# Performance work log

Hardware: AMD Instinct MI355X
Metric: run time of the kernel (lower is better)

Reference implementation:

```python
import jax, jax.numpy as jnp
import numpy as np

B, S, D, E, F = 4, 2048, 1024, 8, 4096


def setup_inputs() -> dict:
    key = jax.random.key(0)
    k1, k2, k3, k4 = jax.random.split(key, 4)
    x = jax.random.normal(k1, (B, S, D), dtype=jnp.float32)
    Wg = jax.random.normal(k2, (D, E), dtype=jnp.float32) / np.sqrt(D).astype(np.float32)
    w1 = jax.random.normal(k3, (E, D, F), dtype=jnp.float32) / np.sqrt(D).astype(np.float32)
    w2 = jax.random.normal(k4, (E, F, D), dtype=jnp.float32) / np.sqrt(F).astype(np.float32)
    return {"x": x, "Wg": Wg, "w1": w1, "w2": w2, "k": 2}


def reference(x, Wg, w1, w2, k):
    # x: [B, S, D] -> flatten tokens
    b, s, d = x.shape
    e = Wg.shape[1]
    xf = x.reshape(-1, d)                      # [T, D]
    t = xf.shape[0]
    logits = xf @ Wg                           # [T, E] gate logits
    topv, topi = jax.lax.top_k(logits, k)      # [T, k]
    # softmax over the top-k logits in float32, cast back (matches torch impl)
    w = jax.nn.softmax(topv.astype(jnp.float32), axis=-1).astype(x.dtype)
    # dense routing matrix [T, E]: weight for selected experts, 0 elsewhere
    route = jnp.zeros((t, e), dtype=x.dtype).at[jnp.arange(t)[:, None], topi].set(w)
    # per-expert FFN: y_e = gelu(x @ w1[e]) @ w2[e]; combine = sum_e route[:,e] * y_e
    out = jnp.zeros_like(xf)
    for ei in range(e):  # small fixed expert count
        h = jax.nn.gelu(xf @ w1[ei])           # [T, F]
        out = out + route[:, ei:ei + 1] * (h @ w2[ei])
    return out.reshape(b, s, d)
```

## Files before the change

kernel.cpp:

```cpp
#include <hip/hip_runtime.h>
#include <stdint.h>

#define T_TOK   8192
#define DMODEL  1024
#define NEXP    8
#define FFN     4096
#define TASSIGN 16384

typedef unsigned short u16;
typedef __attribute__((ext_vector_type(8))) short short8;
typedef __attribute__((ext_vector_type(8))) u16 u16x8;
typedef __attribute__((ext_vector_type(4))) u16 u16x4;
typedef __attribute__((ext_vector_type(4))) float f32x4;

__device__ __forceinline__ float bf2f(u16 u) {
  union { unsigned int i; float f; } v; v.i = ((unsigned int)u) << 16; return v.f;
}
__device__ __forceinline__ u16 f2bf(float f) {
  union { float f; unsigned int i; } v; v.f = f;
  unsigned int x = v.i;
  x += 0x7fffu + ((x >> 16) & 1u);
  return (u16)(x >> 16);
}
__device__ __forceinline__ float gelu_tanh(float x) {
  float z = 0.7978845608028654f * x * (1.0f + 0.044715f * x * x);
  float t = 1.0f - 2.0f / (__expf(2.0f * z) + 1.0f);
  return 0.5f * x * (1.0f + t);
}
__device__ __forceinline__ void async16(const void* g, void* l) {
  __builtin_amdgcn_global_load_lds((__attribute__((address_space(1))) void*)g,
                                   (__attribute__((address_space(3))) void*)l,
                                   16, 0, 0);
}

__global__ void init_kernel(int* __restrict__ meta) {
  if (threadIdx.x < 32) meta[threadIdx.x] = 0;
}

__global__ void gate_kernel(const float* __restrict__ x, const float* __restrict__ Wg,
                            int* __restrict__ topi, float* __restrict__ topw,
                            int* __restrict__ counts, u16* __restrict__ xb) {
  __shared__ float sWg[DMODEL * NEXP];
  int tid = threadIdx.x;
  for (int i = tid; i < DMODEL * NEXP / 4; i += 256)
    ((float4*)sWg)[i] = ((const float4*)Wg)[i];
  __syncthreads();

  int wave = tid >> 6, lane = tid & 63;
  int t = blockIdx.x * 4 + wave;

  float acc[NEXP] = {0, 0, 0, 0, 0, 0, 0, 0};
  const float* xr = x + (size_t)t * DMODEL;
  u16* xbr = xb + (size_t)t * DMODEL;
  for (int d0 = 0; d0 < DMODEL; d0 += 128) {
    int d = d0 + lane * 2;
    float2 xx = *(const float2*)(xr + d);
    *(uint32_t*)(xbr + d) = (uint32_t)f2bf(xx.x) | ((uint32_t)f2bf(xx.y) << 16);
    const float* g0 = sWg + (size_t)d * NEXP;
#pragma unroll
    for (int e = 0; e < NEXP; e++)
      acc[e] += xx.x * g0[e] + xx.y * g0[NEXP + e];
  }
#pragma unroll
  for (int off = 32; off > 0; off >>= 1)
#pragma unroll
    for (int e = 0; e < NEXP; e++)
      acc[e] += __shfl_xor(acc[e], off, 64);

  if (lane == 0) {
    float v0 = -1e30f, v1 = -1e30f; int i0 = 0, i1 = 0;
#pragma unroll
    for (int e = 0; e < NEXP; e++) {
      float v = acc[e];
      if (v > v0) { v1 = v0; i1 = i0; v0 = v; i0 = e; }
      else if (v > v1) { v1 = v; i1 = e; }
    }
    float e1 = __expf(v1 - v0);
    float s = 1.0f / (1.0f + e1);
    topi[t * 2] = i0; topi[t * 2 + 1] = i1;
    topw[t * 2] = s;  topw[t * 2 + 1] = e1 * s;
    atomicAdd(&counts[i0], 1);
    atomicAdd(&counts[i1], 1);
  }
}

__global__ void scan_kernel(const int* __restrict__ counts, int* __restrict__ offsets,
                            int* __restrict__ cursors) {
  if (threadIdx.x == 0) {
    int s = 0;
    for (int e = 0; e < NEXP; e++) { offsets[e] = s; s += counts[e]; }
    offsets[NEXP] = s;
  }
  if (threadIdx.x < NEXP) cursors[threadIdx.x] = 0;
}

__global__ void build_kernel(const int* __restrict__ topi, const int* __restrict__ offsets,
                             int* __restrict__ cursors, int* __restrict__ perm,
                             int* __restrict__ slotrow) {
  int t = blockIdx.x * blockDim.x + threadIdx.x;
  if (t >= T_TOK) return;
#pragma unroll
  for (int s = 0; s < 2; s++) {
    int e = topi[t * 2 + s];
    int p = atomicAdd(&cursors[e], 1);
    int g = offsets[e] + p;
    perm[g] = t;
    slotrow[t * 2 + s] = g;
  }
}

__global__ void transpose_kernel(const float* __restrict__ w1, const float* __restrict__ w2,
                                 u16* __restrict__ w1t, u16* __restrict__ w2t) {
  __shared__ u16 sh[64][72];
  int z = blockIdx.y;
  const float* src; u16* dst; int R, C;
  if (z < 8) { src = w1 + (size_t)z * (DMODEL * FFN); dst = w1t + (size_t)z * (FFN * DMODEL); R = DMODEL; C = FFN; }
  else       { src = w2 + (size_t)(z - 8) * (FFN * DMODEL); dst = w2t + (size_t)(z - 8) * (DMODEL * FFN); R = FFN; C = DMODEL; }
  int tilesC = C >> 6;
  int rt = blockIdx.x / tilesC, ct = blockIdx.x % tilesC;
  int tid = threadIdx.x;
#pragma unroll
  for (int i = 0; i < 2; i++) {
    int idx = i * 256 + tid;
    int r = idx >> 3, c8 = (idx & 7) * 8;
    const float* s = src + (size_t)(rt * 64 + r) * C + ct * 64 + c8;
    float4 v0 = *(const float4*)s, v1 = *(const float4*)(s + 4);
    u16* d = &sh[r][c8];
    d[0] = f2bf(v0.x); d[1] = f2bf(v0.y); d[2] = f2bf(v0.z); d[3] = f2bf(v0.w);
    d[4] = f2bf(v1.x); d[5] = f2bf(v1.y); d[6] = f2bf(v1.z); d[7] = f2bf(v1.w);
  }
  __syncthreads();
#pragma unroll
  for (int i = 0; i < 2; i++) {
    int idx = i * 256 + tid;
    int c = idx >> 3, r8 = (idx & 7) * 8;
    u16x8 v;
#pragma unroll
    for (int j = 0; j < 8; j++) v[j] = sh[r8 + j][c];
    *(u16x8*)(dst + (size_t)(ct * 64 + c) * R + rt * 64 + r8) = v;
  }
}

template <int K, int N, bool GATHER, bool GELU>
__global__ __launch_bounds__(512, 2) void gemm8_kernel(
    const u16* __restrict__ A, const u16* __restrict__ Bt, u16* __restrict__ C,
    const int* __restrict__ offsets, const int* __restrict__ perm) {
  __shared__ u16 S[65536];
  constexpr int NTT = N / 256;
  constexpr int MT  = 32;
  constexpr int NKT = K / 64;
  (void)NTT;

  int p = blockIdx.x;
  int e = p & 7;
  int slot = p >> 3;
  int ntile = slot / MT;
  int mtile = slot % MT;

  int off = offsets[e];
  int nrows = offsets[e + 1] - off;
  if (mtile * 256 >= nrows) return;

  int tid = threadIdx.x;
  int w = tid >> 6, l = tid & 63;
  int lm = l & 15, kq = l >> 4;
  int warp_m = w >> 2, warp_n = w & 3;
  int swz = (lm & 7) << 3;

  int scol8 = ((l & 7) ^ ((l >> 3) & 7)) * 8;
  int rbase = w * 8 + (l >> 3);
  const u16* aptr[2][2];
  const u16* bptr[2][2];
  const u16* bbase = Bt + (size_t)e * ((size_t)N * K);
#pragma unroll
  for (int q = 0; q < 2; q++)
#pragma unroll
    for (int i = 0; i < 2; i++) {
      int rr = rbase + i * 64;
      int rowA = (rr < 64 ? rr : rr + 64) + q * 64;
      int gm = mtile * 256 + rowA;
      int gmc = min(gm, nrows - 1);
      int arow = GATHER ? perm[off + gmc] : (off + gmc);
      aptr[q][i] = A + (size_t)arow * K + scol8;
      int rowB = ((rr >> 5) << 6) + (rr & 31) + q * 32;
      bptr[q][i] = bbase + (size_t)(ntile * 256 + rowB) * K + scol8;
    }
  int arb = w * 8;
  int brb = (w & 3) * 8 + (w >> 2) * 64;
  u16* As_lds = S;
  u16* Bs_lds = S + 32768;

#define STAGE_A(q, buf, kt) do {                                                       \
    async16(aptr[q][0] + (kt) * 64, As_lds + (buf) * 16384 + (arb + (q) * 64) * 64);   \
    async16(aptr[q][1] + (kt) * 64, As_lds + (buf) * 16384 + (arb + 128 + (q) * 64) * 64); \
  } while (0)
#define STAGE_B(q, buf, kt) do {                                                       \
    async16(bptr[q][0] + (kt) * 64, Bs_lds + (buf) * 16384 + (brb + (q) * 32) * 64);   \
    async16(bptr[q][1] + (kt) * 64, Bs_lds + (buf) * 16384 + (brb + 128 + (q) * 32) * 64); \
  } while (0)

  f32x4 acc[8][4];
  f32x4 zero = {0.f, 0.f, 0.f, 0.f};
#pragma unroll
  for (int i = 0; i < 8; i++)
#pragma unroll
    for (int j = 0; j < 4; j++) acc[i][j] = zero;

  short8 af[4][2], b0[2][2], b1[2][2];

#define RD_A(BUF, QM)                                                                  \
  _Pragma("unroll") for (int fi = 0; fi < 4; fi++) {                                   \
    int ml = warp_m * 128 + ((QM) * 4 + fi) * 16 + lm;                                 \
    _Pragma("unroll") for (int ks = 0; ks < 2; ks++)                                   \
      af[fi][ks] = *(const short8*)(As_lds + (BUF) * 16384 + ml * 64 +                 \
                                    ((ks * 32 + kq * 8) ^ swz));                       \
  }
#define RD_B(BUF, QN, BV)                                                              \
  _Pragma("unroll") for (int fj = 0; fj < 2; fj++) {                                   \
    int nl = warp_n * 64 + ((QN) * 2 + fj) * 16 + lm;                                  \
    _Pragma("unroll") for (int ks = 0; ks < 2; ks++)                                   \
      BV[fj][ks] = *(const short8*)(Bs_lds + (BUF) * 16384 + nl * 64 +                 \
                                    ((ks * 32 + kq * 8) ^ swz));                       \
  }
#define MM(QM, QN, BV)                                                                 \
  __builtin_amdgcn_s_barrier();                                                        \
  asm volatile("s_waitcnt lgkmcnt(0)" ::: "memory");                                   \
  __builtin_amdgcn_sched_barrier(0);                                                   \
  __builtin_amdgcn_s_setprio(1);                                                       \
  _Pragma("unroll") for (int fi = 0; fi < 4; fi++)                                     \
    _Pragma("unroll") for (int fj = 0; fj < 2; fj++)                                   \
      _Pragma("unroll") for (int ks = 0; ks < 2; ks++)                                 \
        acc[(QM) * 4 + fi][(QN) * 2 + fj] = __builtin_amdgcn_mfma_f32_16x16x32_bf16(   \
            af[fi][ks], BV[fj][ks], acc[(QM) * 4 + fi][(QN) * 2 + fj], 0, 0, 0);       \
  __builtin_amdgcn_s_setprio(0);

#define TILE(BUF, OBUF, KT1, KT2)                                                      \
  RD_A(BUF, 0) RD_B(BUF, 0, b0) STAGE_B(0, OBUF, KT1);                                 \
  MM(0, 0, b0) __builtin_amdgcn_s_barrier();                                           \
  RD_B(BUF, 1, b1) STAGE_A(0, BUF, KT2);                                               \
  MM(0, 1, b1) __builtin_amdgcn_s_barrier();                                           \
  RD_A(BUF, 1) STAGE_B(1, BUF, KT2);                                                   \
  MM(1, 1, b1) __builtin_amdgcn_s_barrier();                                           \
  RD_B(BUF, 0, b0) STAGE_A(1, BUF, KT2);                                               \
  MM(1, 0, b0)                                                                         \
  asm volatile("s_waitcnt vmcnt(4)" ::: "memory");                                     \
  __builtin_amdgcn_s_barrier();

  STAGE_A(0, 0, 0); STAGE_B(0, 0, 0); STAGE_B(1, 0, 0); STAGE_A(1, 0, 0);
  STAGE_A(0, 1, 1); STAGE_B(1, 1, 1); STAGE_A(1, 1, 1);
  asm volatile("s_waitcnt vmcnt(6)" ::: "memory");
  __builtin_amdgcn_s_barrier();

  for (int it = 0; it < NKT / 2; it++) {
    int kt1 = 2 * it + 1;
    int t2 = min(2 * it + 2, NKT - 1);
    int t3 = min(2 * it + 3, NKT - 1);
    TILE(0, 1, kt1, t2)
    TILE(1, 0, t2, t3)
  }

  asm volatile("s_waitcnt vmcnt(0)" ::: "memory");

#pragma unroll
  for (int fi = 0; fi < 8; fi++) {
    int rowb = mtile * 256 + warp_m * 128 + fi * 16 + kq * 4;
#pragma unroll
    for (int r = 0; r < 4; r++) {
      int row = rowb + r;
      if (row < nrows) {
        u16* crow = C + (size_t)(off + row) * N + ntile * 256 + warp_n * 64 + lm;
#pragma unroll
        for (int fj = 0; fj < 4; fj++) {
          float v = acc[fi][fj][r];
          if (GELU) v = gelu_tanh(v);
          crow[fj * 16] = f2bf(v);
        }
      }
    }
  }
#undef STAGE_A
#undef STAGE_B
#undef RD_A
#undef RD_B
#undef MM
#undef TILE
}

template <int K, int N, bool GATHER, bool GELU>
__global__ __launch_bounds__(256) void gemm_f_kernel(
    const u16* __restrict__ A, const float* __restrict__ B, u16* __restrict__ C,
    const int* __restrict__ offsets, const int* __restrict__ perm) {
  __shared__ u16 As[128 * 32];
  __shared__ u16 Bs[128 * 32];
  int e = blockIdx.z;
  int off = offsets[e];
  int nrows = offsets[e + 1] - off;
  int mtile = blockIdx.y;
  if (mtile * 128 >= nrows) return;
  int ntile = blockIdx.x;

  int tid = threadIdx.x;
  int wave = tid >> 6, lane = tid & 63;

  int rr = tid >> 2;
  int kc = (tid & 3) * 8;
  int m0 = mtile * 128 + rr;
  int mm0 = min(m0, nrows - 1);
  int mm1 = min(m0 + 64, nrows - 1);
  const u16 *arow0, *arow1;
  if (GATHER) {
    arow0 = A + (size_t)perm[off + mm0] * K + kc;
    arow1 = A + (size_t)perm[off + mm1] * K + kc;
  } else {
    arow0 = A + (size_t)(off + mm0) * K + kc;
    arow1 = A + (size_t)(off + mm1) * K + kc;
  }

  int kk2 = (tid >> 4) * 2;
  int n8  = (tid & 15) * 8;
  const float* brow0 = B + (size_t)e * ((size_t)K * N) + (size_t)kk2 * N
                         + (size_t)ntile * 128 + n8;
  const float* brow1 = brow0 + N;

  int wm = (wave >> 1) * 64, wn = (wave & 1) * 64;
  int lm = lane & 15, kq = lane >> 4;

  f32x4 acc[4][4];
  f32x4 zero = {0.f, 0.f, 0.f, 0.f};
#pragma unroll
  for (int i = 0; i < 4; i++)
#pragma unroll
    for (int j = 0; j < 4; j++) acc[i][j] = zero;

  uint32_t* bs32 = (uint32_t*)Bs;
  for (int k0 = 0; k0 < K; k0 += 32) {
    u16x8 av0 = *(const u16x8*)(arow0 + k0);
    u16x8 av1 = *(const u16x8*)(arow1 + k0);
    float4 b00 = *(const float4*)(brow0 + (size_t)k0 * N);
    float4 b01 = *(const float4*)(brow0 + (size_t)k0 * N + 4);
    float4 b10 = *(const float4*)(brow1 + (size_t)k0 * N);
    float4 b11 = *(const float4*)(brow1 + (size_t)k0 * N + 4);
    __syncthreads();
    *(u16x8*)(As + (size_t)rr * 32 + kc) = av0;
    *(u16x8*)(As + (size_t)(rr + 64) * 32 + kc) = av1;
    int wcol = kk2 >> 1;
    bs32[(size_t)(n8 + 0) * 16 + wcol] = (uint32_t)f2bf(b00.x) | ((uint32_t)f2bf(b10.x) << 16);
    bs32[(size_t)(n8 + 1) * 16 + wcol] = (uint32_t)f2bf(b00.y) | ((uint32_t)f2bf(b10.y) << 16);
    bs32[(size_t)(n8 + 2) * 16 + wcol] = (uint32_t)f2bf(b00.z) | ((uint32_t)f2bf(b10.z) << 16);
    bs32[(size_t)(n8 + 3) * 16 + wcol] = (uint32_t)f2bf(b00.w) | ((uint32_t)f2bf(b10.w) << 16);
    bs32[(size_t)(n8 + 4) * 16 + wcol] = (uint32_t)f2bf(b01.x) | ((uint32_t)f2bf(b11.x) << 16);
    bs32[(size_t)(n8 + 5) * 16 + wcol] = (uint32_t)f2bf(b01.y) | ((uint32_t)f2bf(b11.y) << 16);
    bs32[(size_t)(n8 + 6) * 16 + wcol] = (uint32_t)f2bf(b01.z) | ((uint32_t)f2bf(b11.z) << 16);
    bs32[(size_t)(n8 + 7) * 16 + wcol] = (uint32_t)f2bf(b01.w) | ((uint32_t)f2bf(b11.w) << 16);
    __syncthreads();
    short8 a[4], b[4];
#pragma unroll
    for (int i = 0; i < 4; i++) {
      a[i] = *(const short8*)(As + (size_t)(wm + i * 16 + lm) * 32 + kq * 8);
      b[i] = *(const short8*)(Bs + (size_t)(wn + i * 16 + lm) * 32 + kq * 8);
    }
#pragma unroll
    for (int i = 0; i < 4; i++)
#pragma unroll
      for (int j = 0; j < 4; j++)
        acc[i][j] = __builtin_amdgcn_mfma_f32_16x16x32_bf16(a[i], b[j], acc[i][j], 0, 0, 0);
  }

#pragma unroll
  for (int i = 0; i < 4; i++) {
    int rbase = mtile * 128 + wm + i * 16 + kq * 4;
#pragma unroll
    for (int r = 0; r < 4; r++) {
      int row = rbase + r;
      if (row < nrows) {
        u16* crow = C + (size_t)(off + row) * N + ntile * 128 + wn + lm;
#pragma unroll
        for (int j = 0; j < 4; j++) {
          float v = acc[i][j][r];
          if (GELU) v = gelu_tanh(v);
          crow[j * 16] = f2bf(v);
        }
      }
    }
  }
}

__global__ void combine_kernel(const u16* __restrict__ Y, const int* __restrict__ slotrow,
                               const float* __restrict__ topw, float* __restrict__ out) {
  int idx = blockIdx.x * 256 + threadIdx.x;
  int t = idx >> 8;
  int c = (idx & 255) * 4;
  int g0 = slotrow[t * 2], g1 = slotrow[t * 2 + 1];
  float w0 = topw[t * 2], w1 = topw[t * 2 + 1];
  u16x4 y0 = *(const u16x4*)(Y + (size_t)g0 * DMODEL + c);
  u16x4 y1 = *(const u16x4*)(Y + (size_t)g1 * DMODEL + c);
  float4 o;
  o.x = w0 * bf2f(y0[0]) + w1 * bf2f(y1[0]);
  o.y = w0 * bf2f(y0[1]) + w1 * bf2f(y1[1]);
  o.z = w0 * bf2f(y0[2]) + w1 * bf2f(y1[2]);
  o.w = w0 * bf2f(y0[3]) + w1 * bf2f(y1[3]);
  *(float4*)(out + (size_t)t * DMODEL + c) = o;
}

extern "C" void kernel_launch(void* const* d_in, const int* in_sizes, int n_in,
                              void* d_out, int out_size, void* d_ws, size_t ws_size,
                              hipStream_t stream) {
  const float* x  = (const float*)d_in[0];
  const float* Wg = (const float*)d_in[1];
  const float* w1 = (const float*)d_in[2];
  const float* w2 = (const float*)d_in[3];
  float* out = (float*)d_out;

  const size_t SZ_H   = (size_t)TASSIGN * FFN * 2;
  const size_t SZ_W1T = (size_t)NEXP * FFN * DMODEL * 2;
  const size_t SZ_W2T = (size_t)NEXP * DMODEL * FFN * 2;
  const size_t SZ_XB  = (size_t)T_TOK * DMODEL * 2;
  const size_t SZ_Y   = (size_t)TASSIGN * DMODEL * 2;
  const size_t SZ_SMALL = (size_t)TASSIGN * 4 * 4 + 4096;
  const size_t WS_FULL = SZ_H + SZ_W1T + SZ_W2T + SZ_XB + SZ_SMALL;

  uint8_t* ws = (uint8_t*)d_ws;
  bool fast = (ws_size >= WS_FULL);

  size_t o = 0;
  u16* H = (u16*)(ws + o); o += SZ_H;
  u16 *w1t = nullptr, *w2t = nullptr, *Y;
  if (fast) {
    w1t = (u16*)(ws + o); o += SZ_W1T;
    w2t = (u16*)(ws + o); o += SZ_W2T;
    Y = w1t;
  } else {
    Y = (u16*)(ws + o); o += SZ_Y;
  }
  u16* xb = (u16*)(ws + o); o += SZ_XB;
  int*   topi    = (int*)(ws + o);   o += (size_t)TASSIGN * 4;
  float* topw    = (float*)(ws + o); o += (size_t)TASSIGN * 4;
  int*   perm    = (int*)(ws + o);   o += (size_t)TASSIGN * 4;
  int*   slotrow = (int*)(ws + o);   o += (size_t)TASSIGN * 4;
  int*   meta    = (int*)(ws + o);
  int* counts = meta, *offsets = meta + 8, *cursors = meta + 17;

  init_kernel<<<1, 64, 0, stream>>>(meta);
  gate_kernel<<<T_TOK / 4, 256, 0, stream>>>(x, Wg, topi, topw, counts, xb);
  scan_kernel<<<1, 64, 0, stream>>>(counts, offsets, cursors);
  build_kernel<<<T_TOK / 256, 256, 0, stream>>>(topi, offsets, cursors, perm, slotrow);

  if (fast) {
    transpose_kernel<<<dim3(1024, 16), 256, 0, stream>>>(w1, w2, w1t, w2t);
    gemm8_kernel<DMODEL, FFN, true, true>
        <<<NEXP * (FFN / 256) * 32, 512, 0, stream>>>(xb, w1t, H, offsets, perm);
    gemm8_kernel<FFN, DMODEL, false, false>
        <<<NEXP * (DMODEL / 256) * 32, 512, 0, stream>>>(H, w2t, Y, offsets, perm);
  } else {
    gemm_f_kernel<DMODEL, FFN, true, true>
        <<<dim3(FFN / 128, 64, NEXP), 256, 0, stream>>>(xb, w1, H, offsets, perm);
    gemm_f_kernel<FFN, DMODEL, false, false>
        <<<dim3(DMODEL / 128, 64, NEXP), 256, 0, stream>>>(H, w2, Y, offsets, perm);
  }
  combine_kernel<<<(T_TOK * DMODEL / 4) / 256, 256, 0, stream>>>(Y, slotrow, topw, out);
}
```

Baseline: 1.018 ms.

## Restructure expert GEMM into 4-stage pipeline with 32-wide K tiles

```diff
diff --git a/kernel.cpp b/kernel.cpp
--- a/kernel.cpp
+++ b/kernel.cpp
@@ -142,14 +142,12 @@
 }
 
 template <int K, int N, bool GATHER, bool GELU>
-__global__ __launch_bounds__(512, 2) void gemm8_kernel(
+__global__ __launch_bounds__(512, 2) void gemm4_kernel(
     const u16* __restrict__ A, const u16* __restrict__ Bt, u16* __restrict__ C,
     const int* __restrict__ offsets, const int* __restrict__ perm) {
   __shared__ u16 S[65536];
-  constexpr int NTT = N / 256;
   constexpr int MT  = 32;
-  constexpr int NKT = K / 64;
-  (void)NTT;
+  constexpr int NKT = K / 32;
 
   int p = blockIdx.x;
   int e = p & 7;
@@ -165,39 +163,33 @@
   int w = tid >> 6, l = tid & 63;
   int lm = l & 15, kq = l >> 4;
   int warp_m = w >> 2, warp_n = w & 3;
-  int swz = (lm & 7) << 3;
-
-  int scol8 = ((l & 7) ^ ((l >> 3) & 7)) * 8;
-  int rbase = w * 8 + (l >> 3);
-  const u16* aptr[2][2];
-  const u16* bptr[2][2];
+  int rdcol = (kq ^ ((lm >> 1) & 3)) * 8;
+  int scol  = ((l & 3) ^ ((l >> 3) & 3)) * 8;
+
+  const u16* aptr[2];
+  const u16* bptr[2];
   const u16* bbase = Bt + (size_t)e * ((size_t)N * K);
 #pragma unroll
-  for (int q = 0; q < 2; q++)
-#pragma unroll
-    for (int i = 0; i < 2; i++) {
-      int rr = rbase + i * 64;
-      int rowA = (rr < 64 ? rr : rr + 64) + q * 64;
-      int gm = mtile * 256 + rowA;
-      int gmc = min(gm, nrows - 1);
-      int arow = GATHER ? perm[off + gmc] : (off + gmc);
-      aptr[q][i] = A + (size_t)arow * K + scol8;
-      int rowB = ((rr >> 5) << 6) + (rr & 31) + q * 32;
-      bptr[q][i] = bbase + (size_t)(ntile * 256 + rowB) * K + scol8;
-    }
-  int arb = w * 8;
-  int brb = (w & 3) * 8 + (w >> 2) * 64;
-  u16* As_lds = S;
-  u16* Bs_lds = S + 32768;
-
-#define STAGE_A(q, buf, kt) do {                                                       \
-    async16(aptr[q][0] + (kt) * 64, As_lds + (buf) * 16384 + (arb + (q) * 64) * 64);   \
-    async16(aptr[q][1] + (kt) * 64, As_lds + (buf) * 16384 + (arb + 128 + (q) * 64) * 64); \
+  for (int q = 0; q < 2; q++) {
+    int ra = w * 16 + (w >> 2) * 64 + q * 64 + (l >> 2);
+    int gm = min(mtile * 256 + ra, nrows - 1);
+    int arow = GATHER ? perm[off + gm] : (off + gm);
+    aptr[q] = A + (size_t)arow * K + scol;
+  }
+#pragma unroll
+  for (int i = 0; i < 2; i++) {
+    int rb = i * 128 + w * 16 + (l >> 2);
+    bptr[i] = bbase + (size_t)(ntile * 256 + rb) * K + scol;
+  }
+  int adst = (w * 16 + (w >> 2) * 64) * 32;
+  int bdst = 32768 + (w * 16) * 32;
+
+#define STAGE_B(buf, kt) do {                                                  \
+    async16(bptr[0] + (kt) * 32, S + (buf) * 8192 + bdst);                     \
+    async16(bptr[1] + (kt) * 32, S + (buf) * 8192 + bdst + 128 * 32);          \
   } while (0)
-#define STAGE_B(q, buf, kt) do {                                                       \
-    async16(bptr[q][0] + (kt) * 64, Bs_lds + (buf) * 16384 + (brb + (q) * 32) * 64);   \
-    async16(bptr[q][1] + (kt) * 64, Bs_lds + (buf) * 16384 + (brb + 128 + (q) * 32) * 64); \
-  } while (0)
+#define STAGE_A(q, buf, kt)                                                    \
+    async16(aptr[q] + (kt) * 32, S + (buf) * 8192 + adst + (q) * 64 * 32)
 
   f32x4 acc[8][4];
   f32x4 zero = {0.f, 0.f, 0.f, 0.f};
@@ -206,57 +198,54 @@
 #pragma unroll
     for (int j = 0; j < 4; j++) acc[i][j] = zero;
 
-  short8 af[4][2], b0[2][2], b1[2][2];
-
-#define RD_A(BUF, QM)                                                                  \
-  _Pragma("unroll") for (int fi = 0; fi < 4; fi++) {                                   \
-    int ml = warp_m * 128 + ((QM) * 4 + fi) * 16 + lm;                                 \
-    _Pragma("unroll") for (int ks = 0; ks < 2; ks++)                                   \
-      af[fi][ks] = *(const short8*)(As_lds + (BUF) * 16384 + ml * 64 +                 \
-                                    ((ks * 32 + kq * 8) ^ swz));                       \
-  }
-#define RD_B(BUF, QN, BV)                                                              \
-  _Pragma("unroll") for (int fj = 0; fj < 2; fj++) {                                   \
-    int nl = warp_n * 64 + ((QN) * 2 + fj) * 16 + lm;                                  \
-    _Pragma("unroll") for (int ks = 0; ks < 2; ks++)                                   \
-      BV[fj][ks] = *(const short8*)(Bs_lds + (BUF) * 16384 + nl * 64 +                 \
-                                    ((ks * 32 + kq * 8) ^ swz));                       \
-  }
-#define MM(QM, QN, BV)                                                                 \
-  __builtin_amdgcn_s_barrier();                                                        \
-  asm volatile("s_waitcnt lgkmcnt(0)" ::: "memory");                                   \
-  __builtin_amdgcn_sched_barrier(0);                                                   \
-  __builtin_amdgcn_s_setprio(1);                                                       \
-  _Pragma("unroll") for (int fi = 0; fi < 4; fi++)                                     \
-    _Pragma("unroll") for (int fj = 0; fj < 2; fj++)                                   \
-      _Pragma("unroll") for (int ks = 0; ks < 2; ks++)                                 \
-        acc[(QM) * 4 + fi][(QN) * 2 + fj] = __builtin_amdgcn_mfma_f32_16x16x32_bf16(   \
-            af[fi][ks], BV[fj][ks], acc[(QM) * 4 + fi][(QN) * 2 + fj], 0, 0, 0);       \
+  short8 a[4], b[4];
+
+#define RD_A(buf, QM)                                                          \
+  _Pragma("unroll") for (int fi = 0; fi < 4; fi++) {                           \
+    int row = warp_m * 128 + (QM) * 64 + fi * 16 + lm;                         \
+    a[fi] = *(const short8*)(S + (buf) * 8192 + row * 32 + rdcol);             \
+  }
+#define RD_B(buf)                                                              \
+  _Pragma("unroll") for (int nj = 0; nj < 4; nj++) {                           \
+    int row = warp_n * 64 + nj * 16 + lm;                                      \
+    b[nj] = *(const short8*)(S + 32768 + (buf) * 8192 + row * 32 + rdcol);     \
+  }
+#define MM(QM)                                                                 \
+  __builtin_amdgcn_s_barrier();                                                \
+  asm volatile("s_waitcnt lgkmcnt(0)" ::: "memory");                           \
+  __builtin_amdgcn_sched_barrier(0);                                           \
+  __builtin_amdgcn_s_setprio(1);                                               \
+  _Pragma("unroll") for (int fi = 0; fi < 4; fi++)                             \
+    _Pragma("unroll") for (int nj = 0; nj < 4; nj++)                           \
+      acc[(QM) * 4 + fi][nj] = __builtin_amdgcn_mfma_f32_16x16x32_bf16(        \
+          a[fi], b[nj], acc[(QM) * 4 + fi][nj], 0, 0, 0);                      \
   __builtin_amdgcn_s_setprio(0);
 
-#define TILE(BUF, OBUF, KT1, KT2)                                                      \
-  RD_A(BUF, 0) RD_B(BUF, 0, b0) STAGE_B(0, OBUF, KT1);                                 \
-  MM(0, 0, b0) __builtin_amdgcn_s_barrier();                                           \
-  RD_B(BUF, 1, b1) STAGE_A(0, BUF, KT2);                                               \
-  MM(0, 1, b1) __builtin_amdgcn_s_barrier();                                           \
-  RD_A(BUF, 1) STAGE_B(1, BUF, KT2);                                                   \
-  MM(1, 1, b1) __builtin_amdgcn_s_barrier();                                           \
-  RD_B(BUF, 0, b0) STAGE_A(1, BUF, KT2);                                               \
-  MM(1, 0, b0)                                                                         \
-  asm volatile("s_waitcnt vmcnt(4)" ::: "memory");                                     \
+#pragma unroll
+  for (int t0 = 0; t0 < 3; t0++) {
+    int kt = t0 < NKT ? t0 : NKT - 1;
+    STAGE_B(t0 & 3, kt);
+    STAGE_A(0, t0 & 3, kt);
+    STAGE_A(1, t0 & 3, kt);
+  }
+  asm volatile("s_waitcnt vmcnt(9)" ::: "memory");
   __builtin_amdgcn_s_barrier();
 
-  STAGE_A(0, 0, 0); STAGE_B(0, 0, 0); STAGE_B(1, 0, 0); STAGE_A(1, 0, 0);
-  STAGE_A(0, 1, 1); STAGE_B(1, 1, 1); STAGE_A(1, 1, 1);
-  asm volatile("s_waitcnt vmcnt(6)" ::: "memory");
-  __builtin_amdgcn_s_barrier();
-
-  for (int it = 0; it < NKT / 2; it++) {
-    int kt1 = 2 * it + 1;
-    int t2 = min(2 * it + 2, NKT - 1);
-    int t3 = min(2 * it + 3, NKT - 1);
-    TILE(0, 1, kt1, t2)
-    TILE(1, 0, t2, t3)
+  for (int t = 0; t < NKT; t++) {
+    int buf = t & 3, sbuf = (t + 3) & 3;
+    int kt3 = min(t + 3, NKT - 1);
+    RD_B(buf)
+    RD_A(buf, 0)
+    STAGE_B(sbuf, kt3);
+    STAGE_A(0, sbuf, kt3);
+    MM(0)
+    asm volatile("s_waitcnt vmcnt(11)" ::: "memory");
+    __builtin_amdgcn_s_barrier();
+    RD_A(buf, 1)
+    STAGE_A(1, sbuf, kt3);
+    MM(1)
+    asm volatile("s_waitcnt vmcnt(9)" ::: "memory");
+    __builtin_amdgcn_s_barrier();
   }
 
   asm volatile("s_waitcnt vmcnt(0)" ::: "memory");
@@ -283,7 +272,6 @@
 #undef RD_A
 #undef RD_B
 #undef MM
-#undef TILE
 }
 
 template <int K, int N, bool GATHER, bool GELU>
@@ -447,9 +435,9 @@
 
   if (fast) {
     transpose_kernel<<<dim3(1024, 16), 256, 0, stream>>>(w1, w2, w1t, w2t);
-    gemm8_kernel<DMODEL, FFN, true, true>
+    gemm4_kernel<DMODEL, FFN, true, true>
         <<<NEXP * (FFN / 256) * 32, 512, 0, stream>>>(xb, w1t, H, offsets, perm);
-    gemm8_kernel<FFN, DMODEL, false, false>
+    gemm4_kernel<FFN, DMODEL, false, false>
         <<<NEXP * (DMODEL / 256) * 32, 512, 0, stream>>>(H, w2t, Y, offsets, perm);
   } else {
     gemm_f_kernel<DMODEL, FFN, true, true>
```

Result: slower. 1.058 ms (+3.9%).
